# Kernel tuning notes

Hardware: AMD Instinct MI355X
Metric: run time of the kernel (lower is better)

## Reference

```python
import jax, jax.numpy as jnp
import numpy as np

D_MODEL = 1024
N_DIM = 64      # per-head dim; scores scaled by 1/sqrt(n_dim)
N_HEADS = 16
SEQ = 4096
LN_EPS = 1e-5


def setup_inputs() -> dict:
    key = jax.random.key(0)
    ks = jax.random.split(key, 12)
    hd = N_HEADS * N_DIM  # == D_MODEL (required by residual add)
    s = 0.02
    return {
        "embed_word_vec": jax.random.normal(ks[0], (SEQ, D_MODEL), dtype=jnp.float32),
        "attn_mask": jax.random.uniform(ks[1], (SEQ, SEQ)) < 0.1,  # True = masked out
        "wq": jax.random.normal(ks[2], (D_MODEL, hd), dtype=jnp.float32) * s,
        "bq": jnp.zeros((hd,), dtype=jnp.float32),
        "wk": jax.random.normal(ks[3], (D_MODEL, hd), dtype=jnp.float32) * s,
        "bk": jnp.zeros((hd,), dtype=jnp.float32),
        "wv": jax.random.normal(ks[4], (D_MODEL, hd), dtype=jnp.float32) * s,
        "bv": jnp.zeros((hd,), dtype=jnp.float32),
        "wo": jax.random.normal(ks[5], (hd, D_MODEL), dtype=jnp.float32) * s,
        "bo": jnp.zeros((D_MODEL,), dtype=jnp.float32),
        "gamma": jnp.ones((D_MODEL,), dtype=jnp.float32),
        "beta": jnp.zeros((D_MODEL,), dtype=jnp.float32),
    }


def reference(embed_word_vec, attn_mask, wq, bq, wk, bk, wv, bv, wo, bo, gamma, beta):
    x = embed_word_vec                      # [S, d_model]
    q = x @ wq + bq                         # [S, H*D]
    k = x @ wk + bk
    v = x @ wv + bv
    scores = (q @ k.T) / jnp.sqrt(jnp.asarray(N_DIM, dtype=q.dtype))  # [S, S]
    scores = jnp.where(attn_mask, jnp.asarray(-jnp.inf, dtype=scores.dtype), scores)
    attention = jax.nn.softmax(scores, axis=-1)                       # [S, S]
    context = attention @ v + x             # AV + residual, [S, d_model]
    h = context @ wo + bo                   # out projection
    # LayerNorm over last dim
    mu = jnp.mean(h, axis=-1, keepdims=True)
    var = jnp.mean(jnp.square(h - mu), axis=-1, keepdims=True)
    output = (h - mu) * jax.lax.rsqrt(var + LN_EPS) * gamma + beta
    return (output, attention)
```

## Files before the change

kernel.cpp:

```cpp
#include <hip/hip_runtime.h>
#include <hip/hip_bf16.h>
#include <stdint.h>

#define SEQ 4096
#define DM  1024

typedef __attribute__((ext_vector_type(8))) short bf16x8;
typedef __attribute__((ext_vector_type(4))) float f32x4;

template <int V> struct Int { static constexpr int v = V; };

__device__ __forceinline__ short f2bf(float f) {
  union { float f; unsigned int i; } x; x.f = f;
  unsigned int r = x.i + 0x7FFFu + ((x.i >> 16) & 1u);
  return (short)(r >> 16);
}
__device__ __forceinline__ float bf2f(short s) {
  union { unsigned int i; float f; } u;
  u.i = ((unsigned int)(unsigned short)s) << 16;
  return u.f;
}

__device__ __forceinline__ void gload16(const short* g, short* l) {
  __builtin_amdgcn_global_load_lds(
      (const __attribute__((address_space(1))) unsigned int*)g,
      (__attribute__((address_space(3))) unsigned int*)l, 16, 0, 0);
}

__device__ __forceinline__ float wave_max(float v) {
#pragma unroll
  for (int o = 32; o; o >>= 1) v = fmaxf(v, __shfl_xor(v, o));
  return v;
}
__device__ __forceinline__ float wave_sum(float v) {
#pragma unroll
  for (int o = 32; o; o >>= 1) v += __shfl_xor(v, o);
  return v;
}

#define BARRIER() do { asm volatile("" ::: "memory"); \
  __builtin_amdgcn_s_barrier(); asm volatile("" ::: "memory"); } while (0)
#define MF(a, b, c) __builtin_amdgcn_mfma_f32_16x16x32_bf16(a, b, c, 0, 0, 0)

template <int EPI>
__global__ __launch_bounds__(512, 2) void gemm8(
    const short* __restrict__ A, const short* __restrict__ B,
    short* __restrict__ C, short* __restrict__ Cv,
    const float* __restrict__ bias, int Ksplit, int lda, int ldb, int ldc,
    int ldv, float scale, int ntm, int ntn, long csplit, int pc) {
  __shared__ short lds[2][4][8192];
  const int tid = threadIdx.x;
  const int lane = tid & 63;
  const int wid = tid >> 6;
  const int wr = wid >> 2;
  const int wc = wid & 3;
  const int bid = blockIdx.x, nwg = gridDim.x;
  const int chunk = nwg >> 3;
  const int wl = (bid & 7) * chunk + (bid >> 3);
  const int tpg = ntm * ntn;
  const int split = wl / tpg;
  const int r0 = wl - split * tpg;
  const int q = r0 / chunk, i0 = r0 % chunk;
  const int npatch = ntn / pc;
  const int m0 = ((q / npatch) * (chunk / pc) + i0 / pc) * 256;
  const int n0 = ((q % npatch) * pc + i0 % pc) * 256;
  const short* Ab = A + (long)split * Ksplit;
  const short* Bb = B + (long)split * Ksplit;
  short* Co = C + (long)split * csplit;

  const int o0 = tid * 16;
  const int oo = o0 ^ (((o0 >> 7) & 7) << 4);
  const int sr0 = oo >> 7;
  const int sc0 = (oo & 127) >> 1;

  auto stA = [&](int buf, int h, int kt) {
    const short* g = Ab + (long)(m0 + h * 128 + sr0) * lda + kt * 64 + sc0;
    short* l = &lds[buf][h][0] + wid * 512;
    gload16(g, l);
    gload16(g + (long)64 * lda, l + 4096);
  };
  auto stB = [&](int buf, int h, int kt) {
    const short* g = Bb + (long)(n0 + h * 128 + sr0) * ldb + kt * 64 + sc0;
    short* l = &lds[buf][2 + h][0] + wid * 512;
    gload16(g, l);
    gload16(g + (long)64 * ldb, l + 4096);
  };

  const int ll = lane & 15, lh = lane >> 4;
  auto ldaf = [&](int buf, int c, int mm, int kk) {
    const int r = c * 32 + mm * 16 + ll;
    const int off = (r * 64 + kk * 32 + lh * 8) ^ ((r & 7) << 3);
    return *(const bf16x8*)(&lds[buf][wr][0] + off);
  };
  auto ldbf = [&](int buf, int n, int kk) {
    const int r = (wc & 1) * 64 + n * 16 + ll;
    const int off = (r * 64 + kk * 32 + lh * 8) ^ ((r & 7) << 3);
    return *(const bf16x8*)(&lds[buf][2 + (wc >> 1)][0] + off);
  };

  f32x4 acc[8][4];
#pragma unroll
  for (int i = 0; i < 8; i++)
#pragma unroll
    for (int j = 0; j < 4; j++) acc[i][j] = (f32x4){0.f, 0.f, 0.f, 0.f};
  bf16x8 Bf[4][2];

  const int NT = Ksplit >> 6;
  stB(0, 0, 0); stB(0, 1, 0);
  stA(0, 0, 0); stA(0, 1, 0);
  stB(1, 0, 1); stB(1, 1, 1);
  asm volatile("s_waitcnt vmcnt(4)" ::: "memory");
  BARRIER();

  auto phase = [&](auto BUF, auto CC, auto LB, auto BARv, auto&& stg) {
    constexpr int buf = decltype(BUF)::v;
    constexpr int c = decltype(CC)::v;
    if constexpr (decltype(LB)::v != 0) {
#pragma unroll
      for (int n = 0; n < 4; n++) {
        Bf[n][0] = ldbf(buf, n, 0);
        Bf[n][1] = ldbf(buf, n, 1);
      }
    }
    bf16x8 a00 = ldaf(buf, c, 0, 0), a01 = ldaf(buf, c, 0, 1);
    bf16x8 a10 = ldaf(buf, c, 1, 0), a11 = ldaf(buf, c, 1, 1);
    stg();
    if constexpr (decltype(BARv)::v != 0) BARRIER();
    __builtin_amdgcn_s_setprio(1);
#pragma unroll
    for (int n = 0; n < 4; n++) {
      acc[2 * c][n] = MF(a00, Bf[n][0], acc[2 * c][n]);
      acc[2 * c][n] = MF(a01, Bf[n][1], acc[2 * c][n]);
      acc[2 * c + 1][n] = MF(a10, Bf[n][0], acc[2 * c + 1][n]);
      acc[2 * c + 1][n] = MF(a11, Bf[n][1], acc[2 * c + 1][n]);
    }
    __builtin_amdgcn_s_setprio(0);
  };

  for (int t = 0; t < NT; t += 2) {
    const bool nl = (t + 2 < NT);
    phase(Int<0>{}, Int<0>{}, Int<1>{}, Int<0>{},
          [&] { stA(1, 0, t + 1); stA(1, 1, t + 1); });
    phase(Int<0>{}, Int<1>{}, Int<0>{}, Int<1>{}, [] {});
    phase(Int<0>{}, Int<2>{}, Int<0>{}, Int<1>{},
          [&] { if (nl) { stB(0, 0, t + 2); stB(0, 1, t + 2); } });
    phase(Int<0>{}, Int<3>{}, Int<0>{}, Int<1>{}, [] {});
    if (nl) { asm volatile("s_waitcnt vmcnt(4)" ::: "memory"); }
    else    { asm volatile("s_waitcnt vmcnt(0)" ::: "memory"); }
    BARRIER();
    phase(Int<1>{}, Int<0>{}, Int<1>{}, Int<0>{},
          [&] { if (nl) { stA(0, 0, t + 2); stA(0, 1, t + 2); } });
    phase(Int<1>{}, Int<1>{}, Int<0>{}, Int<1>{}, [] {});
    phase(Int<1>{}, Int<2>{}, Int<0>{}, Int<1>{},
          [&] { if (nl) { stB(1, 0, t + 3); stB(1, 1, t + 3); } });
    phase(Int<1>{}, Int<3>{}, Int<0>{}, Int<1>{}, [] {});
    if (nl) {
      asm volatile("s_waitcnt vmcnt(4)" ::: "memory");
      BARRIER();
    }
  }

  const int rb = m0 + wr * 128 + lh * 4;
  const int cb0 = n0 + wc * 64 + ll;
  if (EPI == 3 && n0 >= 2048) {
#pragma unroll
    for (int mi = 0; mi < 8; mi++) {
#pragma unroll
      for (int n = 0; n < 4; n++) {
        const int col = cb0 + n * 16;
        const float bv = bias[col];
        short4 pk;
        pk.x = f2bf(acc[mi][n][0] + bv);
        pk.y = f2bf(acc[mi][n][1] + bv);
        pk.z = f2bf(acc[mi][n][2] + bv);
        pk.w = f2bf(acc[mi][n][3] + bv);
        *(short4*)(Cv + (long)(col - 2048) * ldv + rb + mi * 16) = pk;
      }
    }
    return;
  }
#pragma unroll
  for (int mi = 0; mi < 8; mi++) {
#pragma unroll
    for (int n = 0; n < 4; n++) {
      const int col = cb0 + n * 16;
      float bv = 0.f;
      if (EPI == 1 || EPI == 3) bv = bias[col];
#pragma unroll
      for (int r = 0; r < 4; r++) {
        const int row = rb + mi * 16 + r;
        const long off = (long)row * ldc + col;
        float v = acc[mi][n][r];
        if (EPI == 1 || EPI == 3) v += bv;
        if (EPI == 2) v *= scale;
        Co[off] = f2bf(v);
      }
    }
  }
}


__global__ __launch_bounds__(256) void cvt_f32_to_bf16(
    const float* __restrict__ in, short* __restrict__ out, int n4) {
  int i = blockIdx.x * 256 + threadIdx.x;
  if (i < n4) {
    float4 f = ((const float4*)in)[i];
    short4 o;
    o.x = f2bf(f.x); o.y = f2bf(f.y); o.z = f2bf(f.z); o.w = f2bf(f.w);
    ((short4*)out)[i] = o;
  }
}

__global__ void transpose_w4(const float* __restrict__ s0,
                             const float* __restrict__ s1,
                             const float* __restrict__ s2,
                             const float* __restrict__ s3,
                             short* __restrict__ d0, short* __restrict__ d1,
                             short* __restrict__ d2, short* __restrict__ d3) {
  const int z = blockIdx.z;
  const float* in = z == 0 ? s0 : z == 1 ? s1 : z == 2 ? s2 : s3;
  short* out = z == 0 ? d0 : z == 1 ? d1 : z == 2 ? d2 : d3;
  __shared__ float tile[32][33];
  const int bx = blockIdx.x * 32;
  const int by = blockIdx.y * 32;
  const int tx = threadIdx.x, ty = threadIdx.y;
#pragma unroll
  for (int i = 0; i < 32; i += 8)
    tile[ty + i][tx] = in[(long)(by + ty + i) * 1024 + bx + tx];
  __syncthreads();
#pragma unroll
  for (int i = 0; i < 32; i += 8)
    out[(long)(bx + ty + i) * 1024 + by + tx] = f2bf(tile[tx][ty + i]);
}

__global__ __launch_bounds__(256) void concat_bias(
    const float* __restrict__ bq, const float* __restrict__ bk,
    const float* __restrict__ bv, float* __restrict__ o) {
  int i = blockIdx.x * 256 + threadIdx.x;
  float v = (i < 1024) ? bq[i] : (i < 2048 ? bk[i - 1024] : bv[i - 2048]);
  o[i] = v;
}

__global__ __launch_bounds__(256) void softmax_rows(const short* __restrict__ Sb,
                                                    const int* __restrict__ mask,
                                                    short* __restrict__ Pb) {
  const long row = blockIdx.x;
  const bf16x8* src = (const bf16x8*)(Sb + row * SEQ);
  const int* mrow = mask + row * (long)SEQ;
  bf16x8* dst = (bf16x8*)(Pb + row * SEQ);
  const int tid = threadIdx.x;
  const int wid = tid >> 6, lane = tid & 63;
  bf16x8 a = src[tid], b = src[tid + 256];
  int4 ma0 = *(const int4*)(mrow + tid * 8);
  int4 ma1 = *(const int4*)(mrow + tid * 8 + 4);
  int4 mb0 = *(const int4*)(mrow + 2048 + tid * 8);
  int4 mb1 = *(const int4*)(mrow + 2048 + tid * 8 + 4);
  float v[16];
#pragma unroll
  for (int j = 0; j < 8; j++) { v[j] = bf2f(a[j]); v[8 + j] = bf2f(b[j]); }
  const int* mm0 = (const int*)&ma0;
  const int* mm1 = (const int*)&ma1;
  const int* mm2 = (const int*)&mb0;
  const int* mm3 = (const int*)&mb1;
#pragma unroll
  for (int j = 0; j < 4; j++) {
    if (mm0[j]) v[j] = -INFINITY;
    if (mm1[j]) v[4 + j] = -INFINITY;
    if (mm2[j]) v[8 + j] = -INFINITY;
    if (mm3[j]) v[12 + j] = -INFINITY;
  }
  float mx = -INFINITY;
#pragma unroll
  for (int j = 0; j < 16; j++) mx = fmaxf(mx, v[j]);
  mx = wave_max(mx);
  __shared__ float red[4];
  if (lane == 0) red[wid] = mx;
  __syncthreads();
  mx = fmaxf(fmaxf(red[0], red[1]), fmaxf(red[2], red[3]));
  float sum = 0.f;
#pragma unroll
  for (int j = 0; j < 16; j++) {
    v[j] = __expf(v[j] - mx);
    sum += v[j];
  }
  sum = wave_sum(sum);
  __shared__ float red2[4];
  if (lane == 0) red2[wid] = sum;
  __syncthreads();
  sum = red2[0] + red2[1] + red2[2] + red2[3];
  const float inv = 1.0f / sum;
  bf16x8 o0, o1;
#pragma unroll
  for (int j = 0; j < 8; j++) {
    o0[j] = f2bf(v[j] * inv);
    o1[j] = f2bf(v[8 + j] * inv);
  }
  dst[tid] = o0;
  dst[tid + 256] = o1;
}

__global__ __launch_bounds__(256) void expand_bf16_f32(
    const short* __restrict__ in, float* __restrict__ out) {
  long i = (long)blockIdx.x * 256 + threadIdx.x;
  bf16x8 a = ((const bf16x8*)in)[i];
  float4 lo, hi;
  lo.x = bf2f(a[0]); lo.y = bf2f(a[1]); lo.z = bf2f(a[2]); lo.w = bf2f(a[3]);
  hi.x = bf2f(a[4]); hi.y = bf2f(a[5]); hi.z = bf2f(a[6]); hi.w = bf2f(a[7]);
  ((float4*)out)[2 * i] = lo;
  ((float4*)out)[2 * i + 1] = hi;
}

__global__ __launch_bounds__(256) void reduce_ctx4(
    const short* __restrict__ p, const float* __restrict__ x,
    short* __restrict__ cb) {
  const long i = (long)blockIdx.x * 256 + threadIdx.x;
  bf16x8 a = ((const bf16x8*)p)[i];
  bf16x8 b = ((const bf16x8*)(p + 4194304))[i];
  bf16x8 c = ((const bf16x8*)(p + 8388608))[i];
  bf16x8 d = ((const bf16x8*)(p + 12582912))[i];
  float4 x0 = ((const float4*)x)[2 * i];
  float4 x1 = ((const float4*)x)[2 * i + 1];
  float xs[8] = {x0.x, x0.y, x0.z, x0.w, x1.x, x1.y, x1.z, x1.w};
  bf16x8 o;
#pragma unroll
  for (int j = 0; j < 8; j++)
    o[j] = f2bf(bf2f(a[j]) + bf2f(b[j]) + bf2f(c[j]) + bf2f(d[j]) + xs[j]);
  ((bf16x8*)cb)[i] = o;
}

__global__ __launch_bounds__(256) void ln4(
    const short* __restrict__ ph, const float* __restrict__ bo,
    const float* __restrict__ gamma, const float* __restrict__ beta,
    float* __restrict__ out) {
  const long row = blockIdx.x;
  const int tid = threadIdx.x;
  const int wid = tid >> 6, lane = tid & 63;
  const long base = row * DM + tid * 4;
  short4 p0 = *(const short4*)(ph + base);
  short4 p1 = *(const short4*)(ph + 4194304 + base);
  short4 p2 = *(const short4*)(ph + 8388608 + base);
  short4 p3 = *(const short4*)(ph + 12582912 + base);
  float4 bb = *(const float4*)(bo + tid * 4);
  float v[4];
  v[0] = bf2f(p0.x) + bf2f(p1.x) + bf2f(p2.x) + bf2f(p3.x) + bb.x;
  v[1] = bf2f(p0.y) + bf2f(p1.y) + bf2f(p2.y) + bf2f(p3.y) + bb.y;
  v[2] = bf2f(p0.z) + bf2f(p1.z) + bf2f(p2.z) + bf2f(p3.z) + bb.z;
  v[3] = bf2f(p0.w) + bf2f(p1.w) + bf2f(p2.w) + bf2f(p3.w) + bb.w;
  float s = v[0] + v[1] + v[2] + v[3];
  s = wave_sum(s);
  __shared__ float red[4];
  if (lane == 0) red[wid] = s;
  __syncthreads();
  const float mu = (red[0] + red[1] + red[2] + red[3]) * (1.f / DM);
  float var = 0.f;
#pragma unroll
  for (int j = 0; j < 4; j++) {
    float d = v[j] - mu;
    var += d * d;
  }
  var = wave_sum(var);
  __shared__ float red2[4];
  if (lane == 0) red2[wid] = var;
  __syncthreads();
  var = (red2[0] + red2[1] + red2[2] + red2[3]) * (1.f / DM);
  const float inv = rsqrtf(var + 1e-5f);
  float4 g = *(const float4*)(gamma + tid * 4);
  float4 be = *(const float4*)(beta + tid * 4);
  float4 o;
  o.x = (v[0] - mu) * inv * g.x + be.x;
  o.y = (v[1] - mu) * inv * g.y + be.y;
  o.z = (v[2] - mu) * inv * g.z + be.z;
  o.w = (v[3] - mu) * inv * g.w + be.w;
  *(float4*)(out + base) = o;
}

extern "C" void kernel_launch(void* const* d_in, const int* in_sizes, int n_in,
                              void* d_out, int out_size, void* d_ws,
                              size_t ws_size, hipStream_t stream) {
  const float* x    = (const float*)d_in[0];
  const int* mask   = (const int*)d_in[1];
  const float* wq   = (const float*)d_in[2];
  const float* bq   = (const float*)d_in[3];
  const float* wk   = (const float*)d_in[4];
  const float* bk   = (const float*)d_in[5];
  const float* wv   = (const float*)d_in[6];
  const float* bv   = (const float*)d_in[7];
  const float* wo   = (const float*)d_in[8];
  const float* bo   = (const float*)d_in[9];
  const float* gamma = (const float*)d_in[10];
  const float* beta  = (const float*)d_in[11];

  float* out  = (float*)d_out;
  float* attn = out + 4194304;
  short* Sb   = (short*)attn;
  short* pav  = (short*)attn;
  short* ph   = (short*)(attn + 8388608);
  short* cbuf = (short*)out;

  char* w = (char*)d_ws;
  short* wqkvT = (short*)(w + 0);
  short* woT   = (short*)(w + 6291456);
  short* xb    = (short*)(w + 8388608);
  short* qkv   = (short*)(w + 16777216);
  short* attnb = (short*)(w + 8388608);
  short* vT    = (short*)(w + 41943040);
  float* bqkv  = (float*)(w + 50331648);

  cvt_f32_to_bf16<<<4096, 256, 0, stream>>>(x, xb, 1048576);
  transpose_w4<<<dim3(32, 32, 4), dim3(32, 8), 0, stream>>>(
      wq, wk, wv, wo, wqkvT, wqkvT + 1048576, wqkvT + 2097152, woT);
  concat_bias<<<12, 256, 0, stream>>>(bq, bk, bv, bqkv);

  gemm8<3><<<192, 512, 0, stream>>>(xb, wqkvT, qkv, vT, bqkv,
                                    1024, 1024, 1024, 3072, 4096, 1.f,
                                    16, 12, 0, 6);

  gemm8<2><<<256, 512, 0, stream>>>(qkv, qkv + 1024, Sb, nullptr, nullptr,
                                    1024, 3072, 3072, 4096, 0, 0.125f,
                                    16, 16, 0, 8);

  softmax_rows<<<SEQ, 256, 0, stream>>>(Sb, mask, attnb);

  gemm8<0><<<256, 512, 0, stream>>>(attnb, vT, pav, nullptr, nullptr,
                                    1024, 4096, 4096, 1024, 0, 1.f,
                                    16, 4, 4194304L, 4);

  reduce_ctx4<<<2048, 256, 0, stream>>>(pav, x, cbuf);

  gemm8<0><<<256, 512, 0, stream>>>(cbuf, woT, ph, nullptr, nullptr,
                                    256, 1024, 1024, 1024, 0, 1.f,
                                    16, 4, 4194304L, 4);

  ln4<<<SEQ, 256, 0, stream>>>(ph, bo, gamma, beta, out);

  expand_bf16_f32<<<8192, 256, 0, stream>>>(attnb, attn);
}
```

Measured before the change: 196.8 us.

## Use 32x32x16 MFMA in GEMMs and fuse fp32 attention write into softmax

The GEMM inner loop switches from 16x16x32 bf16 MFMA tiles to 32x32x16 tiles, with new fragment load indexing, accumulator layout and epilogue mapping. This cuts the number of MFMA issues and LDS fragment reads per tile. Separately, when the workspace is large enough, softmax writes the fp32 attention output directly, which removes the final bf16-to-fp32 expand pass. To make room, the score buffer is placed at an offset inside the attention output with a doubled row stride. The fused path depends on ws_size, so whether it runs depends on the harness allocation.

```diff
diff --git a/kernel.cpp b/kernel.cpp
--- a/kernel.cpp
+++ b/kernel.cpp
@@ -6,7 +6,7 @@
 #define DM  1024
 
 typedef __attribute__((ext_vector_type(8))) short bf16x8;
-typedef __attribute__((ext_vector_type(4))) float f32x4;
+typedef __attribute__((ext_vector_type(16))) float f32x16;
 
 template <int V> struct Int { static constexpr int v = V; };
 
@@ -40,7 +40,7 @@
 
 #define BARRIER() do { asm volatile("" ::: "memory"); \
   __builtin_amdgcn_s_barrier(); asm volatile("" ::: "memory"); } while (0)
-#define MF(a, b, c) __builtin_amdgcn_mfma_f32_16x16x32_bf16(a, b, c, 0, 0, 0)
+#define MF32(a, b, c) __builtin_amdgcn_mfma_f32_32x32x16_bf16(a, b, c, 0, 0, 0)
 
 template <int EPI>
 __global__ __launch_bounds__(512, 2) void gemm8(
@@ -86,24 +86,24 @@
     gload16(g + (long)64 * ldb, l + 4096);
   };
 
-  const int ll = lane & 15, lh = lane >> 4;
-  auto ldaf = [&](int buf, int c, int mm, int kk) {
-    const int r = c * 32 + mm * 16 + ll;
-    const int off = (r * 64 + kk * 32 + lh * 8) ^ ((r & 7) << 3);
+  const int lr = lane & 31, l5 = lane >> 5;
+  auto ldaf = [&](int buf, int band, int ks) {
+    const int r = band * 32 + lr;
+    const int off = (r * 64 + ks * 16 + l5 * 8) ^ ((r & 7) << 3);
     return *(const bf16x8*)(&lds[buf][wr][0] + off);
   };
-  auto ldbf = [&](int buf, int n, int kk) {
-    const int r = (wc & 1) * 64 + n * 16 + ll;
-    const int off = (r * 64 + kk * 32 + lh * 8) ^ ((r & 7) << 3);
+  auto ldbf = [&](int buf, int nt, int ks) {
+    const int r = (wc & 1) * 64 + nt * 32 + lr;
+    const int off = (r * 64 + ks * 16 + l5 * 8) ^ ((r & 7) << 3);
     return *(const bf16x8*)(&lds[buf][2 + (wc >> 1)][0] + off);
   };
 
-  f32x4 acc[8][4];
+  f32x16 acc[8];
 #pragma unroll
   for (int i = 0; i < 8; i++)
 #pragma unroll
-    for (int j = 0; j < 4; j++) acc[i][j] = (f32x4){0.f, 0.f, 0.f, 0.f};
-  bf16x8 Bf[4][2];
+    for (int j = 0; j < 16; j++) acc[i][j] = 0.f;
+  bf16x8 Bf[2][4];
 
   const int NT = Ksplit >> 6;
   stB(0, 0, 0); stB(0, 1, 0);
@@ -117,23 +117,23 @@
     constexpr int c = decltype(CC)::v;
     if constexpr (decltype(LB)::v != 0) {
 #pragma unroll
-      for (int n = 0; n < 4; n++) {
-        Bf[n][0] = ldbf(buf, n, 0);
-        Bf[n][1] = ldbf(buf, n, 1);
-      }
+      for (int nt = 0; nt < 2; nt++)
+#pragma unroll
+        for (int ks = 0; ks < 4; ks++) Bf[nt][ks] = ldbf(buf, nt, ks);
     }
-    bf16x8 a00 = ldaf(buf, c, 0, 0), a01 = ldaf(buf, c, 0, 1);
-    bf16x8 a10 = ldaf(buf, c, 1, 0), a11 = ldaf(buf, c, 1, 1);
+    bf16x8 a0 = ldaf(buf, c, 0), a1 = ldaf(buf, c, 1);
+    bf16x8 a2 = ldaf(buf, c, 2), a3 = ldaf(buf, c, 3);
     stg();
     if constexpr (decltype(BARv)::v != 0) BARRIER();
     __builtin_amdgcn_s_setprio(1);
-#pragma unroll
-    for (int n = 0; n < 4; n++) {
-      acc[2 * c][n] = MF(a00, Bf[n][0], acc[2 * c][n]);
-      acc[2 * c][n] = MF(a01, Bf[n][1], acc[2 * c][n]);
-      acc[2 * c + 1][n] = MF(a10, Bf[n][0], acc[2 * c + 1][n]);
-      acc[2 * c + 1][n] = MF(a11, Bf[n][1], acc[2 * c + 1][n]);
-    }
+    acc[2 * c]     = MF32(a0, Bf[0][0], acc[2 * c]);
+    acc[2 * c + 1] = MF32(a0, Bf[1][0], acc[2 * c + 1]);
+    acc[2 * c]     = MF32(a1, Bf[0][1], acc[2 * c]);
+    acc[2 * c + 1] = MF32(a1, Bf[1][1], acc[2 * c + 1]);
+    acc[2 * c]     = MF32(a2, Bf[0][2], acc[2 * c]);
+    acc[2 * c + 1] = MF32(a2, Bf[1][2], acc[2 * c + 1]);
+    acc[2 * c]     = MF32(a3, Bf[0][3], acc[2 * c]);
+    acc[2 * c + 1] = MF32(a3, Bf[1][3], acc[2 * c + 1]);
     __builtin_amdgcn_s_setprio(0);
   };
 
@@ -160,43 +160,43 @@
     }
   }
 
-  const int rb = m0 + wr * 128 + lh * 4;
-  const int cb0 = n0 + wc * 64 + ll;
+  const int rb = m0 + wr * 128 + l5 * 4;
+  const int cb0 = n0 + wc * 64 + lr;
   if (EPI == 3 && n0 >= 2048) {
 #pragma unroll
-    for (int mi = 0; mi < 8; mi++) {
-#pragma unroll
-      for (int n = 0; n < 4; n++) {
-        const int col = cb0 + n * 16;
+    for (int band = 0; band < 4; band++)
+#pragma unroll
+      for (int nt = 0; nt < 2; nt++) {
+        const int col = cb0 + nt * 32;
         const float bv = bias[col];
-        short4 pk;
-        pk.x = f2bf(acc[mi][n][0] + bv);
-        pk.y = f2bf(acc[mi][n][1] + bv);
-        pk.z = f2bf(acc[mi][n][2] + bv);
-        pk.w = f2bf(acc[mi][n][3] + bv);
-        *(short4*)(Cv + (long)(col - 2048) * ldv + rb + mi * 16) = pk;
+#pragma unroll
+        for (int g = 0; g < 4; g++) {
+          short4 pk;
+          pk.x = f2bf(acc[band * 2 + nt][4 * g + 0] + bv);
+          pk.y = f2bf(acc[band * 2 + nt][4 * g + 1] + bv);
+          pk.z = f2bf(acc[band * 2 + nt][4 * g + 2] + bv);
+          pk.w = f2bf(acc[band * 2 + nt][4 * g + 3] + bv);
+          *(short4*)(Cv + (long)(col - 2048) * ldv + rb + band * 32 + g * 8) = pk;
+        }
+      }
+    return;
+  }
+#pragma unroll
+  for (int band = 0; band < 4; band++)
+#pragma unroll
+    for (int nt = 0; nt < 2; nt++) {
+      const int col = cb0 + nt * 32;
+      float bv = 0.f;
+      if (EPI == 1 || EPI == 3) bv = bias[col];
+#pragma unroll
+      for (int r = 0; r < 16; r++) {
+        const int row = rb + band * 32 + (r & 3) + 8 * (r >> 2);
+        float v = acc[band * 2 + nt][r];
+        if (EPI == 1 || EPI == 3) v += bv;
+        if (EPI == 2) v *= scale;
+        Co[(long)row * ldc + col] = f2bf(v);
       }
     }
-    return;
-  }
-#pragma unroll
-  for (int mi = 0; mi < 8; mi++) {
-#pragma unroll
-    for (int n = 0; n < 4; n++) {
-      const int col = cb0 + n * 16;
-      float bv = 0.f;
-      if (EPI == 1 || EPI == 3) bv = bias[col];
-#pragma unroll
-      for (int r = 0; r < 4; r++) {
-        const int row = rb + mi * 16 + r;
-        const long off = (long)row * ldc + col;
-        float v = acc[mi][n][r];
-        if (EPI == 1 || EPI == 3) v += bv;
-        if (EPI == 2) v *= scale;
-        Co[off] = f2bf(v);
-      }
-    }
-  }
 }
 
 
@@ -241,11 +241,14 @@
   o[i] = v;
 }
 
+template <int FUSED>
 __global__ __launch_bounds__(256) void softmax_rows(const short* __restrict__ Sb,
                                                     const int* __restrict__ mask,
-                                                    short* __restrict__ Pb) {
+                                                    short* __restrict__ Pb,
+                                                    float* __restrict__ Af,
+                                                    int ld) {
   const long row = blockIdx.x;
-  const bf16x8* src = (const bf16x8*)(Sb + row * SEQ);
+  const bf16x8* src = (const bf16x8*)(Sb + row * ld);
   const int* mrow = mask + row * (long)SEQ;
   bf16x8* dst = (bf16x8*)(Pb + row * SEQ);
   const int tid = threadIdx.x;
@@ -292,11 +295,20 @@
   bf16x8 o0, o1;
 #pragma unroll
   for (int j = 0; j < 8; j++) {
-    o0[j] = f2bf(v[j] * inv);
-    o1[j] = f2bf(v[8 + j] * inv);
+    v[j] *= inv;
+    v[8 + j] *= inv;
+    o0[j] = f2bf(v[j]);
+    o1[j] = f2bf(v[8 + j]);
   }
   dst[tid] = o0;
   dst[tid + 256] = o1;
+  if (FUSED) {
+    float* orow = Af + row * (long)SEQ;
+    *(float4*)(orow + tid * 4 * 2) = (float4){v[0], v[1], v[2], v[3]};
+    *(float4*)(orow + tid * 4 * 2 + 4) = (float4){v[4], v[5], v[6], v[7]};
+    *(float4*)(orow + 2048 + tid * 8) = (float4){v[8], v[9], v[10], v[11]};
+    *(float4*)(orow + 2048 + tid * 8 + 4) = (float4){v[12], v[13], v[14], v[15]};
+  }
 }
 
 __global__ __launch_bounds__(256) void expand_bf16_f32(
@@ -392,19 +404,22 @@
 
   float* out  = (float*)d_out;
   float* attn = out + 4194304;
-  short* Sb   = (short*)attn;
-  short* pav  = (short*)attn;
-  short* ph   = (short*)(attn + 8388608);
   short* cbuf = (short*)out;
 
   char* w = (char*)d_ws;
+  const bool fused = ws_size >= (size_t)83886080 + 16384;
+  short* Sb   = fused ? (short*)attn + 4096 : (short*)attn;
+  const int ldS = fused ? 8192 : 4096;
+  short* pav  = fused ? (short*)(w + 50331648) : (short*)attn;
+  short* phh  = fused ? pav : (short*)(attn + 8388608);
+  float* bqkv = fused ? (float*)(w + 83886080) : (float*)(w + 50331648);
+
   short* wqkvT = (short*)(w + 0);
   short* woT   = (short*)(w + 6291456);
   short* xb    = (short*)(w + 8388608);
   short* qkv   = (short*)(w + 16777216);
   short* attnb = (short*)(w + 8388608);
   short* vT    = (short*)(w + 41943040);
-  float* bqkv  = (float*)(w + 50331648);
 
   cvt_f32_to_bf16<<<4096, 256, 0, stream>>>(x, xb, 1048576);
   transpose_w4<<<dim3(32, 32, 4), dim3(32, 8), 0, stream>>>(
@@ -416,10 +431,13 @@
                                     16, 12, 0, 6);
 
   gemm8<2><<<256, 512, 0, stream>>>(qkv, qkv + 1024, Sb, nullptr, nullptr,
-                                    1024, 3072, 3072, 4096, 0, 0.125f,
+                                    1024, 3072, 3072, ldS, 0, 0.125f,
                                     16, 16, 0, 8);
 
-  softmax_rows<<<SEQ, 256, 0, stream>>>(Sb, mask, attnb);
+  if (fused)
+    softmax_rows<1><<<SEQ, 256, 0, stream>>>(Sb, mask, attnb, attn, ldS);
+  else
+    softmax_rows<0><<<SEQ, 256, 0, stream>>>(Sb, mask, attnb, attn, ldS);
 
   gemm8<0><<<256, 512, 0, stream>>>(attnb, vT, pav, nullptr, nullptr,
                                     1024, 4096, 4096, 1024, 0, 1.f,
@@ -427,11 +445,11 @@
 
   reduce_ctx4<<<2048, 256, 0, stream>>>(pav, x, cbuf);
 
-  gemm8<0><<<256, 512, 0, stream>>>(cbuf, woT, ph, nullptr, nullptr,
+  gemm8<0><<<256, 512, 0, stream>>>(cbuf, woT, phh, nullptr, nullptr,
                                     256, 1024, 1024, 1024, 0, 1.f,
                                     16, 4, 4194304L, 4);
 
-  ln4<<<SEQ, 256, 0, stream>>>(ph, bo, gamma, beta, out);
-
-  expand_bf16_f32<<<8192, 256, 0, stream>>>(attnb, attn);
-}
+  ln4<<<SEQ, 256, 0, stream>>>(phh, bo, gamma, beta, out);
+
+  if (!fused) expand_bf16_f32<<<8192, 256, 0, stream>>>(attnb, attn);
+}
```

Result: slower. 204.9 us (+4.2%).
